# Optimization experiments

Measured on AMD Instinct MI355X. Metric: run time of the kernel, lower is better.

The kernel has to match this reference:

```python
import jax, jax.numpy as jnp
import numpy as np

D_MODEL = 1024
NUM_HEADS = 16
DEPTH = D_MODEL // NUM_HEADS
B, S = 2, 2048


def setup_inputs() -> dict:
    key = jax.random.key(0)
    ks = jax.random.split(key, 12)
    scale = 1.0 / np.sqrt(D_MODEL)
    inp = {
        "Q": jax.random.normal(ks[0], (B, S, D_MODEL), jnp.float32),
        "K": jax.random.normal(ks[1], (B, S, D_MODEL), jnp.float32),
        "V": jax.random.normal(ks[2], (B, S, D_MODEL), jnp.float32),
        "mask": jnp.zeros((B, 1, 1, S), jnp.float32),  # 1.0 = masked, 0.0 = attend
        "Wq": jax.random.normal(ks[3], (D_MODEL, D_MODEL), jnp.float32) * scale,
        "bq": jnp.zeros((D_MODEL,), jnp.float32),
        "Wk": jax.random.normal(ks[4], (D_MODEL, D_MODEL), jnp.float32) * scale,
        "bk": jnp.zeros((D_MODEL,), jnp.float32),
        "Wv": jax.random.normal(ks[5], (D_MODEL, D_MODEL), jnp.float32) * scale,
        "bv": jnp.zeros((D_MODEL,), jnp.float32),
        "Wo": jax.random.normal(ks[6], (D_MODEL, D_MODEL), jnp.float32) * scale,
        "bo": jnp.zeros((D_MODEL,), jnp.float32),
    }
    return inp


def _split_heads(x):
    b, s, _ = x.shape
    return x.reshape(b, s, NUM_HEADS, DEPTH).transpose(0, 2, 1, 3)  # [b,h,s,d]


def reference(Q, K, V, mask, Wq, bq, Wk, bk, Wv, bv, Wo, bo):
    q = _split_heads(Q @ Wq + bq)
    k = _split_heads(K @ Wk + bk)
    v = _split_heads(V @ Wv + bv)
    scores = jnp.einsum("bhqd,bhkd->bhqk", q, k) / jnp.sqrt(jnp.float32(DEPTH))
    scores = scores + mask * -1e9
    attn = jax.nn.softmax(scores, axis=-1)  # [b,h,q,k]
    out = jnp.einsum("bhqk,bhkd->bhqd", attn, v)
    out = out.transpose(0, 2, 1, 3).reshape(Q.shape[0], -1, D_MODEL)
    out = out @ Wo + bo
    return out, attn
```

## Files before the change

kernel.cpp:

```cpp
#include <hip/hip_runtime.h>

#define D_MODEL 1024
#define NHEADS  16
#define DEPTH   64
#define BB      2
#define SS      2048
#define MROWS   (BB*SS)
#define BHN     (BB*NHEADS)

using f16 = _Float16;
using f16x8 = __attribute__((ext_vector_type(8))) _Float16;
using f32x4 = __attribute__((ext_vector_type(4))) float;

__device__ __forceinline__ void g2l16(const void* g, void* l) {
  __builtin_amdgcn_global_load_lds(
      (const __attribute__((address_space(1))) void*)g,
      (__attribute__((address_space(3))) void*)l, 16, 0, 0);
}

__global__ __launch_bounds__(256) void wtrans(
    const float* __restrict__ w0, const float* __restrict__ w1,
    const float* __restrict__ w2, const float* __restrict__ w3,
    f16* __restrict__ wt) {
  const float* W = blockIdx.z == 0 ? w0 : blockIdx.z == 1 ? w1 : blockIdx.z == 2 ? w2 : w3;
  f16* Wt = wt + (size_t)blockIdx.z * D_MODEL * D_MODEL;
  __shared__ float tile[64][65];
  const int t = threadIdx.x;
  const int bx = blockIdx.x * 64, by = blockIdx.y * 64;
  const int c = t & 63, r0 = t >> 6;
#pragma unroll
  for (int i = 0; i < 16; ++i) {
    int r = r0 + i * 4;
    tile[r][c] = W[(size_t)(by + r) * D_MODEL + bx + c];
  }
  __syncthreads();
#pragma unroll
  for (int i = 0; i < 16; ++i) {
    int r = r0 + i * 4;
    Wt[(size_t)(bx + r) * D_MODEL + by + c] = (f16)tile[c][r];
  }
}

__global__ __launch_bounds__(256) void proj_gemm(
    const float* __restrict__ Q, const float* __restrict__ K, const float* __restrict__ V,
    const f16* __restrict__ Wt,
    const float* __restrict__ bq, const float* __restrict__ bk, const float* __restrict__ bv,
    f16* __restrict__ heads) {
  const int z = blockIdx.z;
  const float* A = z == 0 ? Q : z == 1 ? K : V;
  const f16* Bt = Wt + (size_t)z * D_MODEL * D_MODEL;
  const float* bias = z == 0 ? bq : z == 1 ? bk : bv;
  f16* dst = heads + (size_t)z * MROWS * D_MODEL;

  __shared__ f16 As[128 * 32];
  __shared__ f16 Bs[128 * 32];
  const int t = threadIdx.x, lane = t & 63, w = t >> 6;
  const int m0 = blockIdx.y * 128, n0 = blockIdx.x * 128;
  const int wr = (w >> 1) * 64, wc = (w & 1) * 64;
  f32x4 acc[4][4] = {};

  for (int k0 = 0; k0 < D_MODEL; k0 += 32) {
    __syncthreads();
#pragma unroll
    for (int i = 0; i < 4; ++i) {
      int f = t + i * 256;
      int row = f >> 3, c4 = (f & 7) * 4;
      const float4 v4 = *(const float4*)(A + (size_t)(m0 + row) * D_MODEL + k0 + c4);
      f16* p = &As[row * 32 + c4];
      p[0] = (f16)v4.x; p[1] = (f16)v4.y; p[2] = (f16)v4.z; p[3] = (f16)v4.w;
    }
#pragma unroll
    for (int i = 0; i < 2; ++i) {
      int seg = t + i * 256;
      int row = seg >> 2, c8 = (seg & 3) * 8;
      g2l16(Bt + (size_t)(n0 + row) * D_MODEL + k0 + c8, &Bs[seg * 8]);
    }
    __syncthreads();
    f16x8 af[4], bfr[4];
#pragma unroll
    for (int i = 0; i < 4; ++i)
      af[i] = *(const f16x8*)&As[(wr + i * 16 + (lane & 15)) * 32 + (lane >> 4) * 8];
#pragma unroll
    for (int j = 0; j < 4; ++j)
      bfr[j] = *(const f16x8*)&Bs[(wc + j * 16 + (lane & 15)) * 32 + (lane >> 4) * 8];
#pragma unroll
    for (int i = 0; i < 4; ++i)
#pragma unroll
      for (int j = 0; j < 4; ++j)
        acc[i][j] = __builtin_amdgcn_mfma_f32_16x16x32_f16(af[i], bfr[j], acc[i][j], 0, 0, 0);
  }
#pragma unroll
  for (int i = 0; i < 4; ++i)
#pragma unroll
    for (int j = 0; j < 4; ++j) {
      int n = n0 + wc + j * 16 + (lane & 15);
      float bn = bias[n];
      int h = n >> 6, d = n & 63;
#pragma unroll
      for (int r = 0; r < 4; ++r) {
        int m = m0 + wr + i * 16 + (lane >> 4) * 4 + r;
        int b = m >> 11, s = m & 2047;
        dst[((size_t)(b * NHEADS + h) * SS + s) * DEPTH + d] = (f16)(acc[i][j][r] + bn);
      }
    }
}

__global__ __launch_bounds__(256) void scores_gemm(
    const f16* __restrict__ qh, const f16* __restrict__ kh,
    const float* __restrict__ mask, float* __restrict__ attn) {
  const int bh = blockIdx.z, b = bh >> 4;
  const f16* A = qh + (size_t)bh * SS * DEPTH;
  const f16* Bt = kh + (size_t)bh * SS * DEPTH;
  float* out = attn + (size_t)bh * SS * SS;

  __shared__ f16 As[128 * 32];
  __shared__ f16 Bs[128 * 32];
  const int t = threadIdx.x, lane = t & 63, w = t >> 6;
  const int m0 = blockIdx.y * 128, n0 = blockIdx.x * 128;
  const int wr = (w >> 1) * 64, wc = (w & 1) * 64;
  f32x4 acc[4][4] = {};

  for (int k0 = 0; k0 < DEPTH; k0 += 32) {
    __syncthreads();
#pragma unroll
    for (int i = 0; i < 2; ++i) {
      int seg = t + i * 256;
      int row = seg >> 2, c8 = (seg & 3) * 8;
      g2l16(A + (size_t)(m0 + row) * DEPTH + k0 + c8, &As[seg * 8]);
      g2l16(Bt + (size_t)(n0 + row) * DEPTH + k0 + c8, &Bs[seg * 8]);
    }
    __syncthreads();
    f16x8 af[4], bfr[4];
#pragma unroll
    for (int i = 0; i < 4; ++i)
      af[i] = *(const f16x8*)&As[(wr + i * 16 + (lane & 15)) * 32 + (lane >> 4) * 8];
#pragma unroll
    for (int j = 0; j < 4; ++j)
      bfr[j] = *(const f16x8*)&Bs[(wc + j * 16 + (lane & 15)) * 32 + (lane >> 4) * 8];
#pragma unroll
    for (int i = 0; i < 4; ++i)
#pragma unroll
      for (int j = 0; j < 4; ++j)
        acc[i][j] = __builtin_amdgcn_mfma_f32_16x16x32_f16(af[i], bfr[j], acc[i][j], 0, 0, 0);
  }
#pragma unroll
  for (int i = 0; i < 4; ++i)
#pragma unroll
    for (int j = 0; j < 4; ++j) {
      int n = n0 + wc + j * 16 + (lane & 15);
      float mv = mask[b * SS + n] * (-1e9f);
#pragma unroll
      for (int r = 0; r < 4; ++r) {
        int m = m0 + wr + i * 16 + (lane >> 4) * 4 + r;
        out[(size_t)m * SS + n] = acc[i][j][r] * 0.125f + mv;
      }
    }
}

__global__ __launch_bounds__(256) void softmax_rows(float* __restrict__ attn) {
  float* row = attn + (size_t)blockIdx.x * SS;
  const int t = threadIdx.x;
  float4 a = ((const float4*)row)[t];
  float4 b = ((const float4*)row)[t + 256];
  float mx = fmaxf(fmaxf(fmaxf(a.x, a.y), fmaxf(a.z, a.w)),
                   fmaxf(fmaxf(b.x, b.y), fmaxf(b.z, b.w)));
#pragma unroll
  for (int o = 32; o > 0; o >>= 1) mx = fmaxf(mx, __shfl_xor(mx, o, 64));
  __shared__ float redm[4], reds[4];
  if ((t & 63) == 0) redm[t >> 6] = mx;
  __syncthreads();
  mx = fmaxf(fmaxf(redm[0], redm[1]), fmaxf(redm[2], redm[3]));
  a.x = __expf(a.x - mx); a.y = __expf(a.y - mx); a.z = __expf(a.z - mx); a.w = __expf(a.w - mx);
  b.x = __expf(b.x - mx); b.y = __expf(b.y - mx); b.z = __expf(b.z - mx); b.w = __expf(b.w - mx);
  float sm = a.x + a.y + a.z + a.w + b.x + b.y + b.z + b.w;
#pragma unroll
  for (int o = 32; o > 0; o >>= 1) sm += __shfl_xor(sm, o, 64);
  if ((t & 63) == 0) reds[t >> 6] = sm;
  __syncthreads();
  sm = reds[0] + reds[1] + reds[2] + reds[3];
  float inv = 1.0f / sm;
  a.x *= inv; a.y *= inv; a.z *= inv; a.w *= inv;
  b.x *= inv; b.y *= inv; b.z *= inv; b.w *= inv;
  ((float4*)row)[t] = a;
  ((float4*)row)[t + 256] = b;
}

__global__ __launch_bounds__(256) void pv_gemm(
    const float* __restrict__ attn, const f16* __restrict__ vh, f16* __restrict__ outh) {
  const int bh = blockIdx.y, b = bh >> 4, h = bh & 15;
  const float* A = attn + (size_t)bh * SS * SS;
  const f16* Vh = vh + (size_t)bh * SS * DEPTH;
  const int m0 = blockIdx.x * 256;
  __shared__ f16 As[256 * 32];
  __shared__ f16 Bs[64 * 32];
  const int t = threadIdx.x, lane = t & 63, w = t >> 6;
  f32x4 acc[4][4] = {};

  for (int k0 = 0; k0 < SS; k0 += 32) {
    __syncthreads();
#pragma unroll
    for (int i = 0; i < 8; ++i) {
      int f = t + i * 256;
      int row = f >> 3, c4 = (f & 7) * 4;
      const float4 v4 = *(const float4*)(A + (size_t)(m0 + row) * SS + k0 + c4);
      f16* p = &As[row * 32 + c4];
      p[0] = (f16)v4.x; p[1] = (f16)v4.y; p[2] = (f16)v4.z; p[3] = (f16)v4.w;
    }
#pragma unroll
    for (int i = 0; i < 2; ++i) {
      int f = t + i * 256;
      int kk = f >> 4, d4 = (f & 15) * 4;
      const f16* src = Vh + (size_t)(k0 + kk) * DEPTH + d4;
      f16 v0 = src[0], v1 = src[1], v2 = src[2], v3 = src[3];
      Bs[(d4 + 0) * 32 + kk] = v0; Bs[(d4 + 1) * 32 + kk] = v1;
      Bs[(d4 + 2) * 32 + kk] = v2; Bs[(d4 + 3) * 32 + kk] = v3;
    }
    __syncthreads();
    f16x8 af[4], bfr[4];
#pragma unroll
    for (int i = 0; i < 4; ++i)
      af[i] = *(const f16x8*)&As[(w * 64 + i * 16 + (lane & 15)) * 32 + (lane >> 4) * 8];
#pragma unroll
    for (int j = 0; j < 4; ++j)
      bfr[j] = *(const f16x8*)&Bs[(j * 16 + (lane & 15)) * 32 + (lane >> 4) * 8];
#pragma unroll
    for (int i = 0; i < 4; ++i)
#pragma unroll
      for (int j = 0; j < 4; ++j)
        acc[i][j] = __builtin_amdgcn_mfma_f32_16x16x32_f16(af[i], bfr[j], acc[i][j], 0, 0, 0);
  }
#pragma unroll
  for (int i = 0; i < 4; ++i)
#pragma unroll
    for (int j = 0; j < 4; ++j) {
      int d = j * 16 + (lane & 15);
#pragma unroll
      for (int r = 0; r < 4; ++r) {
        int s = m0 + w * 64 + i * 16 + (lane >> 4) * 4 + r;
        outh[((size_t)b * SS + s) * D_MODEL + h * DEPTH + d] = (f16)acc[i][j][r];
      }
    }
}

__global__ __launch_bounds__(256) void final_gemm(
    const f16* __restrict__ A, const f16* __restrict__ Bt,
    const float* __restrict__ bias, float* __restrict__ out) {
  __shared__ f16 As[128 * 32];
  __shared__ f16 Bs[128 * 32];
  const int t = threadIdx.x, lane = t & 63, w = t >> 6;
  const int m0 = blockIdx.y * 128, n0 = blockIdx.x * 128;
  const int wr = (w >> 1) * 64, wc = (w & 1) * 64;
  f32x4 acc[4][4] = {};

  for (int k0 = 0; k0 < D_MODEL; k0 += 32) {
    __syncthreads();
#pragma unroll
    for (int i = 0; i < 2; ++i) {
      int seg = t + i * 256;
      int row = seg >> 2, c8 = (seg & 3) * 8;
      g2l16(A + (size_t)(m0 + row) * D_MODEL + k0 + c8, &As[seg * 8]);
      g2l16(Bt + (size_t)(n0 + row) * D_MODEL + k0 + c8, &Bs[seg * 8]);
    }
    __syncthreads();
    f16x8 af[4], bfr[4];
#pragma unroll
    for (int i = 0; i < 4; ++i)
      af[i] = *(const f16x8*)&As[(wr + i * 16 + (lane & 15)) * 32 + (lane >> 4) * 8];
#pragma unroll
    for (int j = 0; j < 4; ++j)
      bfr[j] = *(const f16x8*)&Bs[(wc + j * 16 + (lane & 15)) * 32 + (lane >> 4) * 8];
#pragma unroll
    for (int i = 0; i < 4; ++i)
#pragma unroll
      for (int j = 0; j < 4; ++j)
        acc[i][j] = __builtin_amdgcn_mfma_f32_16x16x32_f16(af[i], bfr[j], acc[i][j], 0, 0, 0);
  }
#pragma unroll
  for (int i = 0; i < 4; ++i)
#pragma unroll
    for (int j = 0; j < 4; ++j) {
      int n = n0 + wc + j * 16 + (lane & 15);
      float bn = bias[n];
#pragma unroll
      for (int r = 0; r < 4; ++r) {
        int m = m0 + wr + i * 16 + (lane >> 4) * 4 + r;
        out[(size_t)m * D_MODEL + n] = acc[i][j][r] + bn;
      }
    }
}

extern "C" void kernel_launch(void* const* d_in, const int* in_sizes, int n_in,
                              void* d_out, int out_size, void* d_ws, size_t ws_size,
                              hipStream_t stream) {
  const float* Q    = (const float*)d_in[0];
  const float* K    = (const float*)d_in[1];
  const float* V    = (const float*)d_in[2];
  const float* mask = (const float*)d_in[3];
  const float* Wq   = (const float*)d_in[4];
  const float* bq   = (const float*)d_in[5];
  const float* Wk   = (const float*)d_in[6];
  const float* bk   = (const float*)d_in[7];
  const float* Wv   = (const float*)d_in[8];
  const float* bv   = (const float*)d_in[9];
  const float* Wo   = (const float*)d_in[10];
  const float* bo   = (const float*)d_in[11];

  float* out0 = (float*)d_out;
  float* attn = out0 + (size_t)MROWS * D_MODEL;

  char* ws = (char*)d_ws;
  f16* Wt    = (f16*)ws;
  f16* heads = (f16*)(ws + (size_t)8 * 1024 * 1024);
  f16* outh  = (f16*)(ws + (size_t)32 * 1024 * 1024);
  f16* qh = heads;
  f16* kh = heads + (size_t)MROWS * D_MODEL;
  f16* vh = heads + (size_t)2 * MROWS * D_MODEL;

  wtrans<<<dim3(16, 16, 4), 256, 0, stream>>>(Wq, Wk, Wv, Wo, Wt);
  proj_gemm<<<dim3(8, 32, 3), 256, 0, stream>>>(Q, K, V, Wt, bq, bk, bv, heads);
  scores_gemm<<<dim3(16, 16, BHN), 256, 0, stream>>>(qh, kh, mask, attn);
  softmax_rows<<<dim3(BHN * SS), 256, 0, stream>>>(attn);
  pv_gemm<<<dim3(8, BHN), 256, 0, stream>>>(attn, vh, outh);
  final_gemm<<<dim3(8, 32), 256, 0, stream>>>(outh, Wt + (size_t)3 * D_MODEL * D_MODEL, bo, out0);
}
```

Measured before the change: 1.046 ms.

## Fuse scores, softmax and PV into a two-pass flash-style attention kernel

```diff
diff --git a/kernel.cpp b/kernel.cpp
--- a/kernel.cpp
+++ b/kernel.cpp
@@ -9,6 +9,7 @@
 #define BHN     (BB*NHEADS)
 
 using f16 = _Float16;
+using f16x4 = __attribute__((ext_vector_type(4))) _Float16;
 using f16x8 = __attribute__((ext_vector_type(8))) _Float16;
 using f32x4 = __attribute__((ext_vector_type(4))) float;
 
@@ -105,139 +106,183 @@
     }
 }
 
-__global__ __launch_bounds__(256) void scores_gemm(
+__global__ __launch_bounds__(256) void vtrans(
+    const f16* __restrict__ vh, f16* __restrict__ vt) {
+  const int bh = blockIdx.y;
+  const int n0 = blockIdx.x * 128;
+  const f16* src = vh + (size_t)bh * SS * DEPTH;
+  f16* dst = vt + (size_t)bh * DEPTH * SS;
+  __shared__ f16 tile[128][72];
+  const int t = threadIdx.x;
+#pragma unroll
+  for (int iss = 0; iss < 4; ++iss) {
+    int seg = t + iss * 256;
+    int n = seg >> 3, c = seg & 7;
+    *(f16x8*)&tile[n][c * 8] = *(const f16x8*)(src + (size_t)(n0 + n) * DEPTH + c * 8);
+  }
+  __syncthreads();
+#pragma unroll
+  for (int iss = 0; iss < 4; ++iss) {
+    int seg = t + iss * 256;
+    int d = seg >> 4, c = seg & 15;
+    f16x8 v;
+#pragma unroll
+    for (int e = 0; e < 8; ++e) v[e] = tile[c * 8 + e][d];
+    *(f16x8*)(dst + (size_t)d * SS + n0 + c * 8) = v;
+  }
+}
+
+__global__ __launch_bounds__(256) void attn_fused(
     const f16* __restrict__ qh, const f16* __restrict__ kh,
-    const float* __restrict__ mask, float* __restrict__ attn) {
-  const int bh = blockIdx.z, b = bh >> 4;
-  const f16* A = qh + (size_t)bh * SS * DEPTH;
-  const f16* Bt = kh + (size_t)bh * SS * DEPTH;
-  float* out = attn + (size_t)bh * SS * SS;
-
-  __shared__ f16 As[128 * 32];
-  __shared__ f16 Bs[128 * 32];
+    const f16* __restrict__ vt, const float* __restrict__ mask,
+    float* __restrict__ attn, f16* __restrict__ outh) {
+  const int bh = blockIdx.y, b = bh >> 4, h = bh & 15;
+  const int m0 = blockIdx.x * 128;
+  const f16* Kb = kh + (size_t)bh * SS * DEPTH;
+  const f16* Vb = vt + (size_t)bh * DEPTH * SS;
+  const float* mB = mask + (size_t)b * SS;
+  float* Ab = attn + (size_t)bh * SS * SS;
+
+  __shared__ f16 Ks[2][128 * 64];
+  __shared__ f16 Vs[2][64 * 128];
+
   const int t = threadIdx.x, lane = t & 63, w = t >> 6;
-  const int m0 = blockIdx.y * 128, n0 = blockIdx.x * 128;
-  const int wr = (w >> 1) * 64, wc = (w & 1) * 64;
-  f32x4 acc[4][4] = {};
-
-  for (int k0 = 0; k0 < DEPTH; k0 += 32) {
-    __syncthreads();
-#pragma unroll
-    for (int i = 0; i < 2; ++i) {
-      int seg = t + i * 256;
-      int row = seg >> 2, c8 = (seg & 3) * 8;
-      g2l16(A + (size_t)(m0 + row) * DEPTH + k0 + c8, &As[seg * 8]);
-      g2l16(Bt + (size_t)(n0 + row) * DEPTH + k0 + c8, &Bs[seg * 8]);
-    }
-    __syncthreads();
-    f16x8 af[4], bfr[4];
-#pragma unroll
-    for (int i = 0; i < 4; ++i)
-      af[i] = *(const f16x8*)&As[(wr + i * 16 + (lane & 15)) * 32 + (lane >> 4) * 8];
-#pragma unroll
-    for (int j = 0; j < 4; ++j)
-      bfr[j] = *(const f16x8*)&Bs[(wc + j * 16 + (lane & 15)) * 32 + (lane >> 4) * 8];
-#pragma unroll
-    for (int i = 0; i < 4; ++i)
-#pragma unroll
-      for (int j = 0; j < 4; ++j)
-        acc[i][j] = __builtin_amdgcn_mfma_f32_16x16x32_f16(af[i], bfr[j], acc[i][j], 0, 0, 0);
-  }
-#pragma unroll
-  for (int i = 0; i < 4; ++i)
-#pragma unroll
-    for (int j = 0; j < 4; ++j) {
-      int n = n0 + wc + j * 16 + (lane & 15);
-      float mv = mask[b * SS + n] * (-1e9f);
+  const int l15 = lane & 15, g = lane >> 4;
+
+  f16x8 bq[2][2];
+  {
+    const f16* Qb = qh + (size_t)bh * SS * DEPTH;
+#pragma unroll
+    for (int j = 0; j < 2; ++j)
+#pragma unroll
+      for (int kk = 0; kk < 2; ++kk)
+        bq[j][kk] = *(const f16x8*)(Qb + (size_t)(m0 + w * 32 + j * 16 + l15) * DEPTH + kk * 32 + g * 8);
+  }
+
+  auto stageK = [&](int buf, int ct) {
+#pragma unroll
+    for (int iss = 0; iss < 4; ++iss) {
+      int seg = t + iss * 256;
+      int n = seg >> 3, c = seg & 7;
+      int csrc = c ^ (n & 7);
+      g2l16(Kb + (size_t)(ct * 128 + n) * DEPTH + csrc * 8, &Ks[buf][seg * 8]);
+    }
+  };
+  auto stageV = [&](int buf, int ct) {
+#pragma unroll
+    for (int iss = 0; iss < 4; ++iss) {
+      int seg = t + iss * 256;
+      int d = seg >> 4, c = seg & 15;
+      int csrc = c ^ ((d >> 1) & 7);
+      g2l16(Vb + (size_t)d * SS + ct * 128 + csrc * 8, &Vs[buf][seg * 8]);
+    }
+  };
+  auto qkStep = [&](const f16* ks, f32x4 (&accS)[8][2]) {
+#pragma unroll
+    for (int kk = 0; kk < 2; ++kk) {
+#pragma unroll
+      for (int i = 0; i < 8; ++i) {
+        int n = i * 16 + l15;
+        int c = (g + 4 * kk) ^ (l15 & 7);
+        f16x8 ak = *(const f16x8*)&ks[n * 64 + c * 8];
+#pragma unroll
+        for (int j = 0; j < 2; ++j)
+          accS[i][j] = __builtin_amdgcn_mfma_f32_16x16x32_f16(ak, bq[j][kk], accS[i][j], 0, 0, 0);
+      }
+    }
+  };
+
+  float rm[2] = {-3.0e38f, -3.0e38f}, rs[2] = {0.0f, 0.0f};
+  stageK(0, 0);
+  __syncthreads();
+  for (int ct = 0; ct < 16; ++ct) {
+    const int cur = ct & 1;
+    if (ct < 15) stageK(cur ^ 1, ct + 1);
+    f32x4 accS[8][2] = {};
+    qkStep(Ks[cur], accS);
+#pragma unroll
+    for (int i = 0; i < 8; ++i) {
+      const float4 m4 = *(const float4*)(mB + ct * 128 + i * 16 + g * 4);
+      const float mv[4] = {m4.x * -1e9f, m4.y * -1e9f, m4.z * -1e9f, m4.w * -1e9f};
+#pragma unroll
+      for (int j = 0; j < 2; ++j)
+#pragma unroll
+        for (int r = 0; r < 4; ++r)
+          accS[i][j][r] = accS[i][j][r] * 0.125f + mv[r];
+    }
+#pragma unroll
+    for (int j = 0; j < 2; ++j) {
+      float tm = -3.0e38f;
+#pragma unroll
+      for (int i = 0; i < 8; ++i)
+        tm = fmaxf(tm, fmaxf(fmaxf(accS[i][j][0], accS[i][j][1]),
+                             fmaxf(accS[i][j][2], accS[i][j][3])));
+      tm = fmaxf(tm, __shfl_xor(tm, 16, 64));
+      tm = fmaxf(tm, __shfl_xor(tm, 32, 64));
+      const float mn = fmaxf(rm[j], tm);
+      float ts = 0.0f;
+#pragma unroll
+      for (int i = 0; i < 8; ++i)
+#pragma unroll
+        for (int r = 0; r < 4; ++r)
+          ts += __expf(accS[i][j][r] - mn);
+      ts += __shfl_xor(ts, 16, 64);
+      ts += __shfl_xor(ts, 32, 64);
+      rs[j] = rs[j] * __expf(rm[j] - mn) + ts;
+      rm[j] = mn;
+    }
+    __syncthreads();
+  }
+
+  const float invs[2] = {1.0f / rs[0], 1.0f / rs[1]};
+  f32x4 accO[2][4] = {};
+  stageK(0, 0); stageV(0, 0);
+  __syncthreads();
+  for (int ct = 0; ct < 16; ++ct) {
+    const int cur = ct & 1;
+    if (ct < 15) { stageK(cur ^ 1, ct + 1); stageV(cur ^ 1, ct + 1); }
+    f32x4 accS[8][2] = {};
+    qkStep(Ks[cur], accS);
+    const f16* vs = Vs[cur];
+#pragma unroll
+    for (int i = 0; i < 8; ++i) {
+      const float4 m4 = *(const float4*)(mB + ct * 128 + i * 16 + g * 4);
+      const float mv[4] = {m4.x * -1e9f, m4.y * -1e9f, m4.z * -1e9f, m4.w * -1e9f};
+      f16x4 bv[4];
+#pragma unroll
+      for (int df = 0; df < 4; ++df) {
+        const int d = df * 16 + l15;
+        const int c16 = 2 * i + (g >> 1);
+        const int sw = c16 ^ ((d >> 1) & 7);
+        bv[df] = *(const f16x4*)&vs[d * 128 + sw * 8 + (g & 1) * 4];
+      }
+#pragma unroll
+      for (int j = 0; j < 2; ++j) {
+        float p[4];
+#pragma unroll
+        for (int r = 0; r < 4; ++r)
+          p[r] = __expf(accS[i][j][r] * 0.125f + mv[r] - rm[j]) * invs[j];
+        float4 st; st.x = p[0]; st.y = p[1]; st.z = p[2]; st.w = p[3];
+        *(float4*)(Ab + (size_t)(m0 + w * 32 + j * 16 + l15) * SS + ct * 128 + i * 16 + g * 4) = st;
+        f16x4 pa; pa[0] = (f16)p[0]; pa[1] = (f16)p[1]; pa[2] = (f16)p[2]; pa[3] = (f16)p[3];
+#pragma unroll
+        for (int df = 0; df < 4; ++df)
+          accO[j][df] = __builtin_amdgcn_mfma_f32_16x16x16f16(pa, bv[df], accO[j][df], 0, 0, 0);
+      }
+    }
+    __syncthreads();
+  }
+
+  f16* Ob = outh + (size_t)b * SS * D_MODEL + h * DEPTH;
+#pragma unroll
+  for (int j = 0; j < 2; ++j)
+#pragma unroll
+    for (int df = 0; df < 4; ++df) {
+      const int d = df * 16 + l15;
 #pragma unroll
       for (int r = 0; r < 4; ++r) {
-        int m = m0 + wr + i * 16 + (lane >> 4) * 4 + r;
-        out[(size_t)m * SS + n] = acc[i][j][r] * 0.125f + mv;
-      }
-    }
-}
-
-__global__ __launch_bounds__(256) void softmax_rows(float* __restrict__ attn) {
-  float* row = attn + (size_t)blockIdx.x * SS;
-  const int t = threadIdx.x;
-  float4 a = ((const float4*)row)[t];
-  float4 b = ((const float4*)row)[t + 256];
-  float mx = fmaxf(fmaxf(fmaxf(a.x, a.y), fmaxf(a.z, a.w)),
-                   fmaxf(fmaxf(b.x, b.y), fmaxf(b.z, b.w)));
-#pragma unroll
-  for (int o = 32; o > 0; o >>= 1) mx = fmaxf(mx, __shfl_xor(mx, o, 64));
-  __shared__ float redm[4], reds[4];
-  if ((t & 63) == 0) redm[t >> 6] = mx;
-  __syncthreads();
-  mx = fmaxf(fmaxf(redm[0], redm[1]), fmaxf(redm[2], redm[3]));
-  a.x = __expf(a.x - mx); a.y = __expf(a.y - mx); a.z = __expf(a.z - mx); a.w = __expf(a.w - mx);
-  b.x = __expf(b.x - mx); b.y = __expf(b.y - mx); b.z = __expf(b.z - mx); b.w = __expf(b.w - mx);
-  float sm = a.x + a.y + a.z + a.w + b.x + b.y + b.z + b.w;
-#pragma unroll
-  for (int o = 32; o > 0; o >>= 1) sm += __shfl_xor(sm, o, 64);
-  if ((t & 63) == 0) reds[t >> 6] = sm;
-  __syncthreads();
-  sm = reds[0] + reds[1] + reds[2] + reds[3];
-  float inv = 1.0f / sm;
-  a.x *= inv; a.y *= inv; a.z *= inv; a.w *= inv;
-  b.x *= inv; b.y *= inv; b.z *= inv; b.w *= inv;
-  ((float4*)row)[t] = a;
-  ((float4*)row)[t + 256] = b;
-}
-
-__global__ __launch_bounds__(256) void pv_gemm(
-    const float* __restrict__ attn, const f16* __restrict__ vh, f16* __restrict__ outh) {
-  const int bh = blockIdx.y, b = bh >> 4, h = bh & 15;
-  const float* A = attn + (size_t)bh * SS * SS;
-  const f16* Vh = vh + (size_t)bh * SS * DEPTH;
-  const int m0 = blockIdx.x * 256;
-  __shared__ f16 As[256 * 32];
-  __shared__ f16 Bs[64 * 32];
-  const int t = threadIdx.x, lane = t & 63, w = t >> 6;
-  f32x4 acc[4][4] = {};
-
-  for (int k0 = 0; k0 < SS; k0 += 32) {
-    __syncthreads();
-#pragma unroll
-    for (int i = 0; i < 8; ++i) {
-      int f = t + i * 256;
-      int row = f >> 3, c4 = (f & 7) * 4;
-      const float4 v4 = *(const float4*)(A + (size_t)(m0 + row) * SS + k0 + c4);
-      f16* p = &As[row * 32 + c4];
-      p[0] = (f16)v4.x; p[1] = (f16)v4.y; p[2] = (f16)v4.z; p[3] = (f16)v4.w;
-    }
-#pragma unroll
-    for (int i = 0; i < 2; ++i) {
-      int f = t + i * 256;
-      int kk = f >> 4, d4 = (f & 15) * 4;
-      const f16* src = Vh + (size_t)(k0 + kk) * DEPTH + d4;
-      f16 v0 = src[0], v1 = src[1], v2 = src[2], v3 = src[3];
-      Bs[(d4 + 0) * 32 + kk] = v0; Bs[(d4 + 1) * 32 + kk] = v1;
-      Bs[(d4 + 2) * 32 + kk] = v2; Bs[(d4 + 3) * 32 + kk] = v3;
-    }
-    __syncthreads();
-    f16x8 af[4], bfr[4];
-#pragma unroll
-    for (int i = 0; i < 4; ++i)
-      af[i] = *(const f16x8*)&As[(w * 64 + i * 16 + (lane & 15)) * 32 + (lane >> 4) * 8];
-#pragma unroll
-    for (int j = 0; j < 4; ++j)
-      bfr[j] = *(const f16x8*)&Bs[(j * 16 + (lane & 15)) * 32 + (lane >> 4) * 8];
-#pragma unroll
-    for (int i = 0; i < 4; ++i)
-#pragma unroll
-      for (int j = 0; j < 4; ++j)
-        acc[i][j] = __builtin_amdgcn_mfma_f32_16x16x32_f16(af[i], bfr[j], acc[i][j], 0, 0, 0);
-  }
-#pragma unroll
-  for (int i = 0; i < 4; ++i)
-#pragma unroll
-    for (int j = 0; j < 4; ++j) {
-      int d = j * 16 + (lane & 15);
-#pragma unroll
-      for (int r = 0; r < 4; ++r) {
-        int s = m0 + w * 64 + i * 16 + (lane >> 4) * 4 + r;
-        outh[((size_t)b * SS + s) * D_MODEL + h * DEPTH + d] = (f16)acc[i][j][r];
+        const int s = m0 + w * 32 + j * 16 + g * 4 + r;
+        Ob[(size_t)s * D_MODEL + d] = (f16)accO[j][df][r];
       }
     }
 }
@@ -312,14 +357,14 @@
   f16* Wt    = (f16*)ws;
   f16* heads = (f16*)(ws + (size_t)8 * 1024 * 1024);
   f16* outh  = (f16*)(ws + (size_t)32 * 1024 * 1024);
+  f16* vtr   = (f16*)(ws + (size_t)40 * 1024 * 1024);
   f16* qh = heads;
   f16* kh = heads + (size_t)MROWS * D_MODEL;
   f16* vh = heads + (size_t)2 * MROWS * D_MODEL;
 
   wtrans<<<dim3(16, 16, 4), 256, 0, stream>>>(Wq, Wk, Wv, Wo, Wt);
   proj_gemm<<<dim3(8, 32, 3), 256, 0, stream>>>(Q, K, V, Wt, bq, bk, bv, heads);
-  scores_gemm<<<dim3(16, 16, BHN), 256, 0, stream>>>(qh, kh, mask, attn);
-  softmax_rows<<<dim3(BHN * SS), 256, 0, stream>>>(attn);
-  pv_gemm<<<dim3(8, BHN), 256, 0, stream>>>(attn, vh, outh);
+  vtrans<<<dim3(16, BHN), 256, 0, stream>>>(vh, vtr);
+  attn_fused<<<dim3(16, BHN), 256, 0, stream>>>(qh, kh, vtr, mask, attn, outh);
   final_gemm<<<dim3(8, 32), 256, 0, stream>>>(outh, Wt + (size_t)3 * D_MODEL * D_MODEL, bo, out0);
 }
```

Measured after the change: 850.5 us. -18.7%, faster.
